# Performance work log

Hardware: AMD Instinct MI355X
Metric: run time of the kernel (lower is better)

## Reference

```python
import jax, jax.numpy as jnp
import numpy as np

B, S, D = 4, 2048, 512
H = 8
DK = D // H
DFF = 2048
EPS = 1e-5


def _layernorm(x, g, b):
    mu = jnp.mean(x, axis=-1, keepdims=True)
    var = jnp.mean((x - mu) ** 2, axis=-1, keepdims=True)
    return (x - mu) * jax.lax.rsqrt(var + EPS) * g + b


def setup_inputs() -> dict:
    key = jax.random.key(0)
    ks = jax.random.split(key, 12)
    s = 1.0 / np.sqrt(D)
    sf = 1.0 / np.sqrt(DFF)
    return {
        "x": jax.random.normal(ks[0], (B, S, D), dtype=jnp.float32),
        "Wq": jax.random.uniform(ks[1], (D, D), jnp.float32, -s, s),
        "bq": jnp.zeros((D,), jnp.float32),
        "Wk": jax.random.uniform(ks[2], (D, D), jnp.float32, -s, s),
        "bk": jnp.zeros((D,), jnp.float32),
        "Wv": jax.random.uniform(ks[3], (D, D), jnp.float32, -s, s),
        "bv": jnp.zeros((D,), jnp.float32),
        "Wo": jax.random.uniform(ks[4], (D, D), jnp.float32, -s, s),
        "bo": jnp.zeros((D,), jnp.float32),
        "W1": jax.random.uniform(ks[5], (D, DFF), jnp.float32, -s, s),
        "b1": jnp.zeros((DFF,), jnp.float32),
        "W2": jax.random.uniform(ks[6], (DFF, D), jnp.float32, -sf, sf),
        "b2": jnp.zeros((D,), jnp.float32),
        "g1": jnp.ones((D,), jnp.float32),
        "be1": jnp.zeros((D,), jnp.float32),
        "g2": jnp.ones((D,), jnp.float32),
        "be2": jnp.zeros((D,), jnp.float32),
    }


def reference(x, Wq, bq, Wk, bk, Wv, bv, Wo, bo, W1, b1, W2, b2, g1, be1, g2, be2):
    # Multi-head attention (dropout = identity at eval)
    def heads(v):  # [B,S,D] -> [B,H,S,DK]
        return v.reshape(B, S, H, DK).transpose(0, 2, 1, 3)

    q = heads(x @ Wq + bq)
    k = heads(x @ Wk + bk)
    v = heads(x @ Wv + bv)
    scores = jnp.einsum("bhsd,bhtd->bhst", q, k) / np.sqrt(DK)
    attn = jax.nn.softmax(scores, axis=-1)
    ctx = jnp.einsum("bhst,bhtd->bhsd", attn, v)
    ctx = ctx.transpose(0, 2, 1, 3).reshape(B, S, D)
    attn_out = ctx @ Wo + bo

    x1 = _layernorm(x + attn_out, g1, be1)

    ff = jax.nn.relu(x1 @ W1 + b1) @ W2 + b2
    return _layernorm(x1 + ff, g2, be2)
```

## Files before the change

kernel.cpp:

```cpp
#include <hip/hip_runtime.h>
#include <hip/hip_bf16.h>
#include <stdint.h>

typedef __bf16 bf16;
typedef __attribute__((ext_vector_type(8))) __bf16 bf16x8;
typedef __attribute__((ext_vector_type(4))) float f32x4;

#define DEVI __device__ __forceinline__

constexpr int Bz = 4, Sz = 2048, Dz = 512, Hz = 8, DKz = 64, DFFz = 2048;
constexpr int ROWSz = Bz * Sz;
constexpr float EPSf = 1e-5f;
constexpr float C2f = 0.125f * 1.44269504088896f;

DEVI void load_lds16(void* lds, const void* g) {
  __builtin_amdgcn_global_load_lds(
      (const __attribute__((address_space(1))) void*)(uintptr_t)(g),
      (__attribute__((address_space(3))) void*)(uint32_t)(uintptr_t)(lds),
      16, 0, 0);
}

template <int BM, int BK, int EPI>
__global__ __launch_bounds__(256, BM == 128 ? 4 : 3) void gemm_bt(
    const bf16* __restrict__ A, const bf16* __restrict__ Bt,
    const float* __restrict__ bias, const float* __restrict__ resid,
    const bf16* __restrict__ residb, bf16* __restrict__ aux,
    void* __restrict__ Cout, int M, int N, int K) {
  constexpr int BN = 128;
  constexpr int MI = BM / 32;
  constexpr int RPI = 512 / BK;
  constexpr int AISS = (BM / 4) / RPI;
  constexpr int BISS = 32 / RPI;
  __shared__ alignas(16) bf16 sA[2][BM * BK];
  __shared__ alignas(16) bf16 sB[2][BN * BK];
  const int tid = threadIdx.x;
  const int lane = tid & 63;
  const int wv = tid >> 6;
  const int n0 = blockIdx.x * BN;
  const int m0 = blockIdx.y * BM;

  const int srow = (BK == 32) ? (lane >> 2) : (lane >> 3);
  const int sch = (BK == 32) ? (((lane & 3) ^ (srow & 3)) * 8)
                             : (((lane & 7) ^ (srow & 7)) * 8);
  const bf16* gA = A + (size_t)(m0 + wv * (BM / 4) + srow) * K + sch;
  const bf16* gB = Bt + (size_t)(n0 + wv * 32 + srow) * K + sch;

  const int wm = (wv >> 1) * (BM / 2);
  const int wn = (wv & 1) * 64;
  const int fr = lane & 15;
  const int fq = lane >> 4;

  auto stage = [&](int buf, int k0) {
#pragma unroll
    for (int j = 0; j < AISS; ++j)
      load_lds16(sA[buf] + (wv * (BM / 4) + j * RPI) * BK, gA + (size_t)(j * RPI) * K + k0);
#pragma unroll
    for (int j = 0; j < BISS; ++j)
      load_lds16(sB[buf] + (wv * 32 + j * RPI) * BK, gB + (size_t)(j * RPI) * K + k0);
  };

  f32x4 acc[MI][4] = {};

  stage(0, 0);
  __syncthreads();

  const int niter = K / BK;
  for (int it = 0; it < niter; ++it) {
    const int cur = it & 1;
    if (it + 1 < niter) stage(cur ^ 1, (it + 1) * BK);
#pragma unroll
    for (int kk = 0; kk < BK / 32; ++kk) {
      const int fc = (BK == 32) ? ((fq ^ (fr & 3)) * 8)
                                : (((4 * kk + fq) ^ (fr & 7)) * 8);
      bf16x8 af[MI], bfr[4];
#pragma unroll
      for (int i = 0; i < MI; ++i)
        af[i] = *(const bf16x8*)(sA[cur] + (wm + i * 16 + fr) * BK + fc);
#pragma unroll
      for (int j = 0; j < 4; ++j)
        bfr[j] = *(const bf16x8*)(sB[cur] + (wn + j * 16 + fr) * BK + fc);
#pragma unroll
      for (int i = 0; i < MI; ++i)
#pragma unroll
        for (int j = 0; j < 4; ++j)
          acc[i][j] = __builtin_amdgcn_mfma_f32_16x16x32_bf16(af[i], bfr[j], acc[i][j], 0, 0, 0);
    }
    __syncthreads();
  }

#pragma unroll
  for (int i = 0; i < MI; ++i) {
#pragma unroll
    for (int j = 0; j < 4; ++j) {
      const int col = n0 + wn + j * 16 + fr;
      const float bv = bias[col];
      if (EPI == 3 && col >= 1024) {
        const int row0 = m0 + wm + i * 16 + fq * 4;
        const int hh = (col - 1024) >> 6, dk = (col - 1024) & 63;
        const int bb = row0 >> 11, s0 = row0 & 2047;
        bf16 pv[4];
#pragma unroll
        for (int r = 0; r < 4; ++r) pv[r] = (bf16)(acc[i][j][r] + bv);
        *(uint2*)(aux + (size_t)((bb * 8 + hh) * 64 + dk) * 2048 + s0) = *(const uint2*)pv;
      } else {
#pragma unroll
        for (int r = 0; r < 4; ++r) {
          const int row = m0 + wm + i * 16 + fq * 4 + r;
          const size_t idx = (size_t)row * N + col;
          float v = acc[i][j][r] + bv;
          if (EPI == 1) {
            ((bf16*)Cout)[idx] = (bf16)(v + resid[idx]);
          } else if (EPI == 2) {
            ((bf16*)Cout)[idx] = (bf16)(v > 0.f ? v : 0.f);
          } else if (EPI == 3) {
            ((bf16*)Cout)[idx] = (bf16)(col < 512 ? v * C2f : v);
          } else {
            ((bf16*)Cout)[idx] = (bf16)(v + (float)residb[idx]);
          }
        }
      }
    }
  }
}

__global__ __launch_bounds__(256, 2) void flash_attn(
    const bf16* __restrict__ qkv, const bf16* __restrict__ Vt,
    bf16* __restrict__ ctx) {
  const int bid = blockIdx.x;
  const int qt = bid & 15;
  const int h = (bid >> 4) & 7;
  const int b = bid >> 7;
  const int q0 = qt * 128;
  const int tid = threadIdx.x, lane = tid & 63, wv = tid >> 6;
  const int fr = lane & 15, fq = lane >> 4;
  const int xsw = fr & 7;

  __shared__ alignas(16) bf16 sK[2][64 * 64];
  __shared__ alignas(16) bf16 sV[2][64 * 64];
  __shared__ alignas(16) bf16 sP[128 * 64];

  const int srow = lane >> 3;
  const int scol = ((lane & 7) ^ srow) * 8;

  const bf16* gQ = qkv + (size_t)(b * Sz + q0 + wv * 32 + srow) * 1536 + h * 64 + scol;
  const bf16* gK = qkv + (size_t)(b * Sz + wv * 16 + srow) * 1536 + 512 + h * 64 + scol;
  const bf16* gV = Vt + (size_t)((b * 8 + h) * 64 + wv * 16 + srow) * Sz + scol;

#pragma unroll
  for (int i = 0; i < 4; ++i)
    load_lds16(sP + (wv * 32 + i * 8) * 64, gQ + (size_t)(i * 8) * 1536);
  load_lds16(sK[0] + (wv * 16 + 0) * 64, gK);
  load_lds16(sK[0] + (wv * 16 + 8) * 64, gK + (size_t)8 * 1536);
  load_lds16(sV[0] + (wv * 16 + 0) * 64, gV);
  load_lds16(sV[0] + (wv * 16 + 8) * 64, gV + (size_t)8 * Sz);
  asm volatile("s_waitcnt vmcnt(0)" ::: "memory");
  __syncthreads();

  const int colc0 = (fq ^ xsw) * 8;
  const int colc1 = ((fq + 4) ^ xsw) * 8;
  int pcol[4], qsrc[4];
#pragma unroll
  for (int j = 0; j < 4; ++j)
    pcol[j] = (((fq + 4 * j) >> 1) ^ xsw) * 8 + (fq & 1) * 4;
#pragma unroll
  for (int r = 0; r < 4; ++r) qsrc[r] = (fq * 4 + r) | (lane & 48);

  bf16x8 qb[2][2];
#pragma unroll
  for (int s = 0; s < 2; ++s) {
    qb[s][0] = *(const bf16x8*)(sP + (wv * 32 + s * 16 + fr) * 64 + colc0);
    qb[s][1] = *(const bf16x8*)(sP + (wv * 32 + s * 16 + fr) * 64 + colc1);
  }
  asm volatile("s_waitcnt lgkmcnt(0)" ::: "memory");

  float l_part[2] = {0.f, 0.f};
  f32x4 acc_o[2][4] = {};

  for (int it = 0; it < 32; ++it) {
    const int cur = it & 1;
    if (it + 1 < 32) {
      const int nxt = cur ^ 1;
      const size_t t1 = (size_t)(it + 1) * 64;
      load_lds16(sK[nxt] + (wv * 16 + 0) * 64, gK + t1 * 1536);
      load_lds16(sK[nxt] + (wv * 16 + 8) * 64, gK + (t1 + 8) * 1536);
      load_lds16(sV[nxt] + (wv * 16 + 0) * 64, gV + t1);
      load_lds16(sV[nxt] + (wv * 16 + 8) * 64, gV + (size_t)8 * Sz + t1);
    }

    bf16x8 kf[2][4];
#pragma unroll
    for (int j = 0; j < 4; ++j) {
      kf[0][j] = *(const bf16x8*)(sK[cur] + (j * 16 + fr) * 64 + colc0);
      kf[1][j] = *(const bf16x8*)(sK[cur] + (j * 16 + fr) * 64 + colc1);
    }
    f32x4 sc[2][4] = {};
#pragma unroll
    for (int s = 0; s < 2; ++s)
#pragma unroll
      for (int kk = 0; kk < 2; ++kk)
#pragma unroll
        for (int j = 0; j < 4; ++j)
          sc[s][j] = __builtin_amdgcn_mfma_f32_16x16x32_bf16(kf[kk][j], qb[s][kk], sc[s][j], 0, 0, 0);

#pragma unroll
    for (int s = 0; s < 2; ++s) {
      float rs = 0.f;
#pragma unroll
      for (int j = 0; j < 4; ++j) {
        float e0 = __builtin_amdgcn_exp2f(sc[s][j][0]);
        float e1 = __builtin_amdgcn_exp2f(sc[s][j][1]);
        float e2 = __builtin_amdgcn_exp2f(sc[s][j][2]);
        float e3 = __builtin_amdgcn_exp2f(sc[s][j][3]);
        rs += (e0 + e1) + (e2 + e3);
        bf16 pt[4] = {(bf16)e0, (bf16)e1, (bf16)e2, (bf16)e3};
        *(uint2*)(sP + (wv * 32 + s * 16 + fr) * 64 + pcol[j]) = *(const uint2*)pt;
      }
      l_part[s] += rs;
    }
    asm volatile("s_waitcnt lgkmcnt(0)" ::: "memory");

    bf16x8 vf[2][4];
#pragma unroll
    for (int j = 0; j < 4; ++j) {
      vf[0][j] = *(const bf16x8*)(sV[cur] + (j * 16 + fr) * 64 + colc0);
      vf[1][j] = *(const bf16x8*)(sV[cur] + (j * 16 + fr) * 64 + colc1);
    }
#pragma unroll
    for (int s = 0; s < 2; ++s)
#pragma unroll
      for (int kk = 0; kk < 2; ++kk) {
        bf16x8 ap = *(const bf16x8*)(sP + (wv * 32 + s * 16 + fr) * 64 + (kk ? colc1 : colc0));
#pragma unroll
        for (int j = 0; j < 4; ++j)
          acc_o[s][j] = __builtin_amdgcn_mfma_f32_16x16x32_bf16(ap, vf[kk][j], acc_o[s][j], 0, 0, 0);
      }
    __syncthreads();
  }

#pragma unroll
  for (int s = 0; s < 2; ++s) {
    float l = l_part[s];
    l += __shfl_xor(l, 16, 64);
    l += __shfl_xor(l, 32, 64);
    float rl[4];
#pragma unroll
    for (int r = 0; r < 4; ++r) rl[r] = 1.0f / __shfl(l, qsrc[r], 64);
#pragma unroll
    for (int j = 0; j < 4; ++j)
#pragma unroll
      for (int r = 0; r < 4; ++r) {
        const int row = b * Sz + q0 + wv * 32 + s * 16 + fq * 4 + r;
        const int col = h * 64 + j * 16 + fr;
        ctx[(size_t)row * Dz + col] = (bf16)(acc_o[s][j][r] * rl[r]);
      }
  }
}

template <int OUT_F32>
__global__ __launch_bounds__(256) void layer_norm_k(
    const bf16* __restrict__ y, const float* __restrict__ g,
    const float* __restrict__ be, void* __restrict__ out) {
  const int row = blockIdx.x * 4 + (threadIdx.x >> 6);
  const int lane = threadIdx.x & 63;
  const int col = lane * 8;
  bf16x8 hv = *(const bf16x8*)(y + (size_t)row * Dz + col);
  float v[8];
  float s = 0.f, ss = 0.f;
#pragma unroll
  for (int i = 0; i < 8; ++i) {
    v[i] = (float)hv[i];
    s += v[i];
    ss += v[i] * v[i];
  }
#pragma unroll
  for (int o = 1; o < 64; o <<= 1) {
    s += __shfl_xor(s, o, 64);
    ss += __shfl_xor(ss, o, 64);
  }
  const float mu = s * (1.0f / Dz);
  const float rstd = rsqrtf(ss * (1.0f / Dz) - mu * mu + EPSf);
  const float4* g4 = (const float4*)(g + col);
  const float4* b4 = (const float4*)(be + col);
  float4 ga = g4[0], gb = g4[1], ba = b4[0], bb = b4[1];
  float o8[8];
  o8[0] = (v[0] - mu) * rstd * ga.x + ba.x;
  o8[1] = (v[1] - mu) * rstd * ga.y + ba.y;
  o8[2] = (v[2] - mu) * rstd * ga.z + ba.z;
  o8[3] = (v[3] - mu) * rstd * ga.w + ba.w;
  o8[4] = (v[4] - mu) * rstd * gb.x + bb.x;
  o8[5] = (v[5] - mu) * rstd * gb.y + bb.y;
  o8[6] = (v[6] - mu) * rstd * gb.z + bb.z;
  o8[7] = (v[7] - mu) * rstd * gb.w + bb.w;
  if (OUT_F32) {
    float4* of = (float4*)((float*)out + (size_t)row * Dz + col);
    of[0] = make_float4(o8[0], o8[1], o8[2], o8[3]);
    of[1] = make_float4(o8[4], o8[5], o8[6], o8[7]);
  } else {
    bf16 ob[8];
#pragma unroll
    for (int i = 0; i < 8; ++i) ob[i] = (bf16)o8[i];
    *(uint4*)((bf16*)out + (size_t)row * Dz + col) = *(const uint4*)ob;
  }
}

__global__ __launch_bounds__(256) void prep_all(
    const float* __restrict__ Wq, const float* __restrict__ Wk,
    const float* __restrict__ Wv, const float* __restrict__ Wo,
    const float* __restrict__ W1, const float* __restrict__ W2,
    const float* __restrict__ bq, const float* __restrict__ bk,
    const float* __restrict__ bv, const float* __restrict__ x,
    bf16* __restrict__ WqkvT, bf16* __restrict__ WoT,
    bf16* __restrict__ W1T, bf16* __restrict__ W2T,
    float* __restrict__ bqkv, bf16* __restrict__ xb) {
  __shared__ float tile[64][65];
  const int blk = blockIdx.x;
  const int t = threadIdx.x;
  if (blk < 768) {
    const float* W;
    bf16* Wt;
    int K, N, local;
    if (blk < 64)       { W = Wq; Wt = WqkvT;                       K = 512;  N = 512;  local = blk; }
    else if (blk < 128) { W = Wk; Wt = WqkvT + (size_t)512 * 512;   K = 512;  N = 512;  local = blk - 64; }
    else if (blk < 192) { W = Wv; Wt = WqkvT + (size_t)1024 * 512;  K = 512;  N = 512;  local = blk - 128; }
    else if (blk < 256) { W = Wo; Wt = WoT;                         K = 512;  N = 512;  local = blk - 192; }
    else if (blk < 512) { W = W1; Wt = W1T;                         K = 512;  N = 2048; local = blk - 256; }
    else                { W = W2; Wt = W2T;                         K = 2048; N = 512;  local = blk - 512; }
    const int kt = K / 64;
    const int k0 = (local % kt) * 64, n0 = (local / kt) * 64;
    const int r = t >> 2, c = (t & 3) * 16;
    const float* src = W + (size_t)(k0 + r) * N + n0 + c;
#pragma unroll
    for (int i = 0; i < 4; ++i) {
      float4 v = ((const float4*)src)[i];
      tile[r][c + i * 4 + 0] = v.x;
      tile[r][c + i * 4 + 1] = v.y;
      tile[r][c + i * 4 + 2] = v.z;
      tile[r][c + i * 4 + 3] = v.w;
    }
    __syncthreads();
    union { bf16 hh[16]; uint4 u[2]; } pk;
#pragma unroll
    for (int i = 0; i < 16; ++i) pk.hh[i] = (bf16)tile[c + i][r];
    uint4* dst = (uint4*)(Wt + (size_t)(n0 + r) * K + k0 + c);
    dst[0] = pk.u[0];
    dst[1] = pk.u[1];
  } else if (blk == 768) {
    for (int i = t; i < 1536; i += 256)
      bqkv[i] = i < 512 ? bq[i] : (i < 1024 ? bk[i - 512] : bv[i - 1024]);
  } else {
    const int local = blk - 769;
#pragma unroll
    for (int k = 0; k < 4; ++k) {
      const int i = local * 1024 + k * 256 + t;
      float4 v = ((const float4*)x)[i];
      bf16 tv[4] = {(bf16)v.x, (bf16)v.y, (bf16)v.z, (bf16)v.w};
      ((uint2*)xb)[i] = *(const uint2*)tv;
    }
  }
}

extern "C" void kernel_launch(void* const* d_in, const int* in_sizes, int n_in,
                              void* d_out, int out_size, void* d_ws, size_t ws_size,
                              hipStream_t stream) {
  const float* x   = (const float*)d_in[0];
  const float* Wq  = (const float*)d_in[1];
  const float* bq  = (const float*)d_in[2];
  const float* Wk  = (const float*)d_in[3];
  const float* bk  = (const float*)d_in[4];
  const float* Wv  = (const float*)d_in[5];
  const float* bvp = (const float*)d_in[6];
  const float* Wo  = (const float*)d_in[7];
  const float* bo  = (const float*)d_in[8];
  const float* W1  = (const float*)d_in[9];
  const float* b1  = (const float*)d_in[10];
  const float* W2  = (const float*)d_in[11];
  const float* b2  = (const float*)d_in[12];
  const float* g1  = (const float*)d_in[13];
  const float* be1 = (const float*)d_in[14];
  const float* g2  = (const float*)d_in[15];
  const float* be2 = (const float*)d_in[16];

  char* ws = (char*)d_ws;
  size_t off = 0;
  auto alloc = [&](size_t bytes) -> void* {
    void* p = ws + off;
    off += (bytes + 255) & ~(size_t)255;
    return p;
  };
  bf16*  WqkvT = (bf16*)alloc((size_t)1536 * 512 * 2);
  float* bqkv  = (float*)alloc(1536 * 4);
  bf16*  WoT   = (bf16*)alloc((size_t)512 * 512 * 2);
  bf16*  W1T   = (bf16*)alloc((size_t)2048 * 512 * 2);
  bf16*  W2T   = (bf16*)alloc((size_t)512 * 2048 * 2);
  bf16*  xb    = (bf16*)alloc((size_t)ROWSz * 512 * 2);
  bf16*  qkv   = (bf16*)alloc((size_t)ROWSz * 1536 * 2);
  bf16*  Vt    = (bf16*)alloc((size_t)32 * 64 * 2048 * 2);
  bf16*  ctx   = (bf16*)alloc((size_t)ROWSz * 512 * 2);
  bf16*  y1    = (bf16*)alloc((size_t)ROWSz * 512 * 2);
  bf16*  x1b   = (bf16*)alloc((size_t)ROWSz * 512 * 2);
  bf16*  hbuf  = qkv;
  bf16*  y2    = y1;

  prep_all<<<dim3(1793), 256, 0, stream>>>(Wq, Wk, Wv, Wo, W1, W2, bq, bk, bvp, x,
                                           WqkvT, WoT, W1T, W2T, bqkv, xb);

  gemm_bt<128, 32, 3><<<dim3(12, 64), 256, 0, stream>>>(xb, WqkvT, bqkv, nullptr, nullptr, Vt, qkv, ROWSz, 1536, 512);
  flash_attn<<<dim3(512), 256, 0, stream>>>(qkv, Vt, ctx);
  gemm_bt<64, 64, 4><<<dim3(4, 128), 256, 0, stream>>>(ctx, WoT, bo, nullptr, xb, nullptr, y1, ROWSz, 512, 512);
  layer_norm_k<0><<<dim3(2048), 256, 0, stream>>>(y1, g1, be1, x1b);
  gemm_bt<128, 32, 2><<<dim3(16, 64), 256, 0, stream>>>(x1b, W1T, b1, nullptr, nullptr, nullptr, hbuf, ROWSz, 2048, 512);
  gemm_bt<64, 64, 4><<<dim3(4, 128), 256, 0, stream>>>(hbuf, W2T, b2, nullptr, x1b, nullptr, y2, ROWSz, 512, 2048);
  layer_norm_k<1><<<dim3(2048), 256, 0, stream>>>(y2, g2, be2, d_out);
}
```

Measured before the change: 246.3 us.

## Keep attention probabilities in registers via permlane swaps and triple-buffer K/V

The flash attention kernel stops staging the exp'd probabilities through LDS. It repacks them into MFMA A-operand layout in registers with v_permlane32/16_swap, which removes the sP buffer, its LDS writes and reads, and an lgkmcnt wait. K/V loads move to a three-stage ring with prefetch distance two, using partial vmcnt waits and raw s_barrier instead of __syncthreads. s_setprio is raised around the MFMA blocks. LDS use stays about the same, but the correctness of the register transpose and the barrier/waitcnt ordering is delicate.

```diff
diff --git a/kernel.cpp b/kernel.cpp
--- a/kernel.cpp
+++ b/kernel.cpp
@@ -18,6 +18,13 @@
       (const __attribute__((address_space(1))) void*)(uintptr_t)(g),
       (__attribute__((address_space(3))) void*)(uint32_t)(uintptr_t)(lds),
       16, 0, 0);
+}
+
+DEVI void permswap32(unsigned& x, unsigned& y) {
+  asm("v_permlane32_swap_b32 %0, %1" : "+v"(x), "+v"(y));
+}
+DEVI void permswap16(unsigned& x, unsigned& y) {
+  asm("v_permlane16_swap_b32 %0, %1" : "+v"(x), "+v"(y));
 }
 
 template <int BM, int BK, int EPI>
@@ -135,9 +142,8 @@
   const int fr = lane & 15, fq = lane >> 4;
   const int xsw = fr & 7;
 
-  __shared__ alignas(16) bf16 sK[2][64 * 64];
-  __shared__ alignas(16) bf16 sV[2][64 * 64];
-  __shared__ alignas(16) bf16 sP[128 * 64];
+  __shared__ alignas(16) bf16 sK[3][64 * 64];
+  __shared__ alignas(16) bf16 sV[3][64 * 64];
 
   const int srow = lane >> 3;
   const int scol = ((lane & 7) ^ srow) * 8;
@@ -146,45 +152,50 @@
   const bf16* gK = qkv + (size_t)(b * Sz + wv * 16 + srow) * 1536 + 512 + h * 64 + scol;
   const bf16* gV = Vt + (size_t)((b * 8 + h) * 64 + wv * 16 + srow) * Sz + scol;
 
+  bf16* sQ = (bf16*)sK;
 #pragma unroll
   for (int i = 0; i < 4; ++i)
-    load_lds16(sP + (wv * 32 + i * 8) * 64, gQ + (size_t)(i * 8) * 1536);
-  load_lds16(sK[0] + (wv * 16 + 0) * 64, gK);
-  load_lds16(sK[0] + (wv * 16 + 8) * 64, gK + (size_t)8 * 1536);
-  load_lds16(sV[0] + (wv * 16 + 0) * 64, gV);
-  load_lds16(sV[0] + (wv * 16 + 8) * 64, gV + (size_t)8 * Sz);
+    load_lds16(sQ + (wv * 32 + i * 8) * 64, gQ + (size_t)(i * 8) * 1536);
   asm volatile("s_waitcnt vmcnt(0)" ::: "memory");
-  __syncthreads();
 
   const int colc0 = (fq ^ xsw) * 8;
   const int colc1 = ((fq + 4) ^ xsw) * 8;
-  int pcol[4], qsrc[4];
-#pragma unroll
-  for (int j = 0; j < 4; ++j)
-    pcol[j] = (((fq + 4 * j) >> 1) ^ xsw) * 8 + (fq & 1) * 4;
+  int qsrc[4];
 #pragma unroll
   for (int r = 0; r < 4; ++r) qsrc[r] = (fq * 4 + r) | (lane & 48);
 
   bf16x8 qb[2][2];
 #pragma unroll
   for (int s = 0; s < 2; ++s) {
-    qb[s][0] = *(const bf16x8*)(sP + (wv * 32 + s * 16 + fr) * 64 + colc0);
-    qb[s][1] = *(const bf16x8*)(sP + (wv * 32 + s * 16 + fr) * 64 + colc1);
+    qb[s][0] = *(const bf16x8*)(sQ + (wv * 32 + s * 16 + fr) * 64 + colc0);
+    qb[s][1] = *(const bf16x8*)(sQ + (wv * 32 + s * 16 + fr) * 64 + colc1);
   }
   asm volatile("s_waitcnt lgkmcnt(0)" ::: "memory");
+  __syncthreads();
+
+  auto stage = [&](int buf, int t) {
+    const size_t t0r = (size_t)t * 64;
+    load_lds16(sK[buf] + (wv * 16 + 0) * 64, gK + t0r * 1536);
+    load_lds16(sK[buf] + (wv * 16 + 8) * 64, gK + (t0r + 8) * 1536);
+    load_lds16(sV[buf] + (wv * 16 + 0) * 64, gV + t0r);
+    load_lds16(sV[buf] + (wv * 16 + 8) * 64, gV + (size_t)8 * Sz + t0r);
+  };
+
+  stage(0, 0);
+  stage(1, 1);
+  asm volatile("s_waitcnt vmcnt(4)" ::: "memory");
+  __builtin_amdgcn_s_barrier();
+  asm volatile("" ::: "memory");
 
   float l_part[2] = {0.f, 0.f};
   f32x4 acc_o[2][4] = {};
+  int cur = 0;
 
   for (int it = 0; it < 32; ++it) {
-    const int cur = it & 1;
-    if (it + 1 < 32) {
-      const int nxt = cur ^ 1;
-      const size_t t1 = (size_t)(it + 1) * 64;
-      load_lds16(sK[nxt] + (wv * 16 + 0) * 64, gK + t1 * 1536);
-      load_lds16(sK[nxt] + (wv * 16 + 8) * 64, gK + (t1 + 8) * 1536);
-      load_lds16(sV[nxt] + (wv * 16 + 0) * 64, gV + t1);
-      load_lds16(sV[nxt] + (wv * 16 + 8) * 64, gV + (size_t)8 * Sz + t1);
+    if (it + 2 < 32) {
+      int nb = cur + 2;
+      if (nb >= 3) nb -= 3;
+      stage(nb, it + 2);
     }
 
     bf16x8 kf[2][4];
@@ -194,6 +205,7 @@
       kf[1][j] = *(const bf16x8*)(sK[cur] + (j * 16 + fr) * 64 + colc1);
     }
     f32x4 sc[2][4] = {};
+    __builtin_amdgcn_s_setprio(1);
 #pragma unroll
     for (int s = 0; s < 2; ++s)
 #pragma unroll
@@ -201,9 +213,12 @@
 #pragma unroll
         for (int j = 0; j < 4; ++j)
           sc[s][j] = __builtin_amdgcn_mfma_f32_16x16x32_bf16(kf[kk][j], qb[s][kk], sc[s][j], 0, 0, 0);
-
+    __builtin_amdgcn_s_setprio(0);
+
+    bf16x8 pa[2][2];
 #pragma unroll
     for (int s = 0; s < 2; ++s) {
+      unsigned c0[4], c1[4];
       float rs = 0.f;
 #pragma unroll
       for (int j = 0; j < 4; ++j) {
@@ -212,12 +227,26 @@
         float e2 = __builtin_amdgcn_exp2f(sc[s][j][2]);
         float e3 = __builtin_amdgcn_exp2f(sc[s][j][3]);
         rs += (e0 + e1) + (e2 + e3);
-        bf16 pt[4] = {(bf16)e0, (bf16)e1, (bf16)e2, (bf16)e3};
-        *(uint2*)(sP + (wv * 32 + s * 16 + fr) * 64 + pcol[j]) = *(const uint2*)pt;
+        union { bf16 hh[2]; unsigned u; } pka, pkb;
+        pka.hh[0] = (bf16)e0; pka.hh[1] = (bf16)e1;
+        pkb.hh[0] = (bf16)e2; pkb.hh[1] = (bf16)e3;
+        c0[j] = pka.u;
+        c1[j] = pkb.u;
       }
       l_part[s] += rs;
-    }
-    asm volatile("s_waitcnt lgkmcnt(0)" ::: "memory");
+#pragma unroll
+      for (int kk = 0; kk < 2; ++kk) {
+        unsigned x0 = c0[2 * kk], y0 = c0[2 * kk + 1];
+        permswap32(x0, y0);
+        permswap16(x0, y0);
+        unsigned x1 = c1[2 * kk], y1 = c1[2 * kk + 1];
+        permswap32(x1, y1);
+        permswap16(x1, y1);
+        union { unsigned u[4]; bf16x8 v; } pk;
+        pk.u[0] = x0; pk.u[1] = x1; pk.u[2] = y0; pk.u[3] = y1;
+        pa[s][kk] = pk.v;
+      }
+    }
 
     bf16x8 vf[2][4];
 #pragma unroll
@@ -225,16 +254,23 @@
       vf[0][j] = *(const bf16x8*)(sV[cur] + (j * 16 + fr) * 64 + colc0);
       vf[1][j] = *(const bf16x8*)(sV[cur] + (j * 16 + fr) * 64 + colc1);
     }
+    __builtin_amdgcn_s_setprio(1);
 #pragma unroll
     for (int s = 0; s < 2; ++s)
 #pragma unroll
-      for (int kk = 0; kk < 2; ++kk) {
-        bf16x8 ap = *(const bf16x8*)(sP + (wv * 32 + s * 16 + fr) * 64 + (kk ? colc1 : colc0));
+      for (int kk = 0; kk < 2; ++kk)
 #pragma unroll
         for (int j = 0; j < 4; ++j)
-          acc_o[s][j] = __builtin_amdgcn_mfma_f32_16x16x32_bf16(ap, vf[kk][j], acc_o[s][j], 0, 0, 0);
-      }
-    __syncthreads();
+          acc_o[s][j] = __builtin_amdgcn_mfma_f32_16x16x32_bf16(pa[s][kk], vf[kk][j], acc_o[s][j], 0, 0, 0);
+    __builtin_amdgcn_s_setprio(0);
+
+    if (it < 31) {
+      if (it < 30) asm volatile("s_waitcnt vmcnt(4)" ::: "memory");
+      else         asm volatile("s_waitcnt vmcnt(0)" ::: "memory");
+      __builtin_amdgcn_s_barrier();
+      asm volatile("" ::: "memory");
+    }
+    cur = cur == 2 ? 0 : cur + 1;
   }
 
 #pragma unroll
```

Measured after the change: 251.0 us. No clear change (+1.9%).
